# Kernel tuning notes

Measured on AMD Instinct MI355X. Metric: run time of the kernel, lower is better.

The kernel has to match this reference:

```python
import jax, jax.numpy as jnp
import numpy as np

EPS = 1e-07


def _pairwise_iou_xyxy(pred, tgt):
    # pred: [P,4], tgt: [T,4] in (x1,y1,x2,y2) form -> [P,T] IoU
    lt = jnp.maximum(pred[:, None, :2], tgt[None, :, :2])   # [P,T,2]
    rb = jnp.minimum(pred[:, None, 2:], tgt[None, :, 2:])   # [P,T,2]
    wh = jnp.clip(rb - lt, 0.0)                             # [P,T,2]
    inter = wh[..., 0] * wh[..., 1]                         # [P,T]
    pa = (pred[:, 2] - pred[:, 0]) * (pred[:, 3] - pred[:, 1])  # [P]
    ta = (tgt[:, 2] - tgt[:, 0]) * (tgt[:, 3] - tgt[:, 1])      # [T]
    union = pa[:, None] + ta[None, :] - inter
    return inter / (union + EPS)


def setup_inputs() -> dict:
    key = jax.random.key(0)
    k1, k2 = jax.random.split(key)
    pred_boxes = jax.random.uniform(k1, (8192, 4), dtype=jnp.float32)
    target_boxes = jax.random.uniform(k2, (4096, 4), dtype=jnp.float32)
    return {"pred_boxes": pred_boxes, "target_boxes": target_boxes}


def reference(pred_boxes, target_boxes):
    num_preds = pred_boxes.shape[0]
    num_targets = target_boxes.shape[0]
    if num_preds != num_targets:
        pairwise_ious = _pairwise_iou_xyxy(pred_boxes, target_boxes)  # [P,T]
        indices = jnp.argmax(pairwise_ious, axis=1)                    # [P]
        target_boxes = target_boxes[indices]                           # [P,4]

    # DIoU part interprets boxes as (cx, cy, w, h) -- faithful to the original
    pred_centers, pred_sizes = pred_boxes[:, :2], pred_boxes[:, 2:]
    tgt_centers, tgt_sizes = target_boxes[:, :2], target_boxes[:, 2:]

    pred_lt = pred_centers - pred_sizes / 2
    pred_rb = pred_centers + pred_sizes / 2
    tgt_lt = tgt_centers - tgt_sizes / 2
    tgt_rb = tgt_centers + tgt_sizes / 2

    inter_wh = jnp.clip(jnp.minimum(pred_rb, tgt_rb) - jnp.maximum(pred_lt, tgt_lt), 0.0)
    inter_area = inter_wh[:, 0] * inter_wh[:, 1]
    pred_area = pred_sizes[:, 0] * pred_sizes[:, 1]
    tgt_area = tgt_sizes[:, 0] * tgt_sizes[:, 1]
    iou = inter_area / (pred_area + tgt_area - inter_area + EPS)

    center_distance = jnp.sum((pred_centers - tgt_centers) ** 2, axis=1)
    enc_wh = jnp.maximum(pred_rb, tgt_rb) - jnp.minimum(pred_lt, tgt_lt)
    enc_diag = jnp.sum(enc_wh ** 2, axis=1)

    diou = iou - center_distance / (enc_diag + EPS)
    return 1.0 - jnp.mean(diou)
```

## Files before the change

kernel.cpp:

```cpp
#include <hip/hip_runtime.h>

#define EPS 1e-7f

constexpr int NPRED  = 8192;
constexpr int NTGT   = 4096;
constexpr int BLOCK  = 256;
constexpr int PW     = 4;
constexpr int PPB    = 16;
constexpr int TSPLIT = 8;
constexpr int TCHUNK = NTGT / TSPLIT;
constexpr int GRID_P = NPRED / PPB;
constexpr int GRID   = GRID_P * TSPLIT;

__device__ __forceinline__ unsigned sortable_key(float f) {
  unsigned b = __float_as_uint(f);
  return (b & 0x80000000u) ? ~b : (b | 0x80000000u);
}

__global__ __launch_bounds__(BLOCK, 8)
void diou_argmax(const float4* __restrict__ pred,
                 const float4* __restrict__ tgt,
                 unsigned long long* __restrict__ pk) {
  __shared__ float4 sT[TCHUNK];
  const int lane  = threadIdx.x & 63;
  const int wave  = threadIdx.x >> 6;
  const int pblk  = blockIdx.x % GRID_P;
  const int tq    = blockIdx.x / GRID_P;
  const int tbase = tq * TCHUNK;
  const int pbase = pblk * PPB + wave * PW;

  for (int t = threadIdx.x; t < TCHUNK; t += BLOCK) sT[t] = tgt[tbase + t];

  float4 p[PW];
  float  paeps[PW];
  float  bestV[PW];
  int    bestI[PW];
#pragma unroll
  for (int i = 0; i < PW; ++i) {
    p[i]     = pred[pbase + i];
    paeps[i] = (p[i].z - p[i].x) * (p[i].w - p[i].y) + EPS;
    bestV[i] = -INFINITY;
    bestI[i] = 0;
  }
  __syncthreads();

#pragma unroll 4
  for (int t0 = 0; t0 < TCHUNK; t0 += 64) {
    const int t = t0 + lane;
    float4 tb = sT[t];
    float  ta = (tb.z - tb.x) * (tb.w - tb.y);
#pragma unroll
    for (int i = 0; i < PW; ++i) {
      float w = fminf(p[i].z, tb.z) - fmaxf(p[i].x, tb.x);
      float h = fminf(p[i].w, tb.w) - fmaxf(p[i].y, tb.y);
      w = fmaxf(w, 0.f);
      h = fmaxf(h, 0.f);
      float inter = w * h;
      float denom = (paeps[i] + ta) - inter;
      float iou   = inter * __builtin_amdgcn_rcpf(denom);
      iou += 0.0f;
      if (iou > bestV[i]) { bestV[i] = iou; bestI[i] = t; }
    }
  }

#pragma unroll
  for (int i = 0; i < PW; ++i) {
    float v  = bestV[i];
    int   ix = bestI[i];
    for (int off = 32; off > 0; off >>= 1) {
      float ov = __shfl_down(v, off, 64);
      int   oi = __shfl_down(ix, off, 64);
      if (ov > v || (ov == v && oi < ix)) { v = ov; ix = oi; }
    }
    if (lane == 0) {
      unsigned long long packed =
          ((unsigned long long)sortable_key(v) << 32) |
          (unsigned)(NTGT - 1 - (tbase + ix));
      atomicMax(&pk[pbase + i], packed);
    }
  }
}

__global__ __launch_bounds__(1024)
void diou_gather_finalize(const float4* __restrict__ pred,
                          const float4* __restrict__ tgt,
                          const unsigned long long* __restrict__ pk,
                          float* __restrict__ out) {
  __shared__ float sP[16];
  const int tid  = threadIdx.x;
  const int lane = tid & 63;

  float v = 0.f;
  for (int j = tid; j < NPRED; j += 1024) {
    float4 p  = pred[j];
    int    ix = NTGT - 1 - (int)(unsigned)(pk[j] & 0xFFFFFFFFu);
    float4 t  = tgt[ix];

    float phw = 0.5f * p.z, phh = 0.5f * p.w;
    float thw = 0.5f * t.z, thh = 0.5f * t.w;
    float pltx = p.x - phw, plty = p.y - phh;
    float prbx = p.x + phw, prby = p.y + phh;
    float tltx = t.x - thw, tlty = t.y - thh;
    float trbx = t.x + thw, trby = t.y + thh;

    float iw = fmaxf(fminf(prbx, trbx) - fmaxf(pltx, tltx), 0.f);
    float ih = fmaxf(fminf(prby, trby) - fmaxf(plty, tlty), 0.f);
    float inter = iw * ih;
    float parea = p.z * p.w;
    float tarea = t.z * t.w;
    float iou   = inter / (parea + tarea - inter + EPS);

    float dx = p.x - t.x, dy = p.y - t.y;
    float cd = dx * dx + dy * dy;

    float ew = fmaxf(prbx, trbx) - fminf(pltx, tltx);
    float eh = fmaxf(prby, trby) - fminf(plty, tlty);
    float diag = ew * ew + eh * eh;

    v += iou - cd / (diag + EPS);
  }

  for (int off = 32; off > 0; off >>= 1) v += __shfl_down(v, off, 64);
  if (lane == 0) sP[tid >> 6] = v;
  __syncthreads();
  if (tid == 0) {
    float s = 0.f;
#pragma unroll
    for (int i = 0; i < 16; ++i) s += sP[i];
    out[0] = 1.f - s * (1.f / (float)NPRED);
  }
}

extern "C" void kernel_launch(void* const* d_in, const int* in_sizes, int n_in,
                              void* d_out, int out_size, void* d_ws, size_t ws_size,
                              hipStream_t stream) {
  const float4* pred = (const float4*)d_in[0];
  const float4* tgt  = (const float4*)d_in[1];
  unsigned long long* pk = (unsigned long long*)d_ws;

  hipMemsetAsync(pk, 0, NPRED * sizeof(unsigned long long), stream);
  diou_argmax<<<GRID, BLOCK, 0, stream>>>(pred, tgt, pk);
  diou_gather_finalize<<<1, 1024, 0, stream>>>(pred, tgt, pk, (float*)d_out);
}
```

Measured before the change: 83.57 us.

## Fuse argmax with DIoU gather, drop target split and atomics

```diff
diff --git a/kernel.cpp b/kernel.cpp
--- a/kernel.cpp
+++ b/kernel.cpp
@@ -2,100 +2,65 @@
 
 #define EPS 1e-7f
 
-constexpr int NPRED  = 8192;
-constexpr int NTGT   = 4096;
-constexpr int BLOCK  = 256;
-constexpr int PW     = 4;
-constexpr int PPB    = 16;
-constexpr int TSPLIT = 8;
-constexpr int TCHUNK = NTGT / TSPLIT;
-constexpr int GRID_P = NPRED / PPB;
-constexpr int GRID   = GRID_P * TSPLIT;
-
-__device__ __forceinline__ unsigned sortable_key(float f) {
-  unsigned b = __float_as_uint(f);
-  return (b & 0x80000000u) ? ~b : (b | 0x80000000u);
-}
+constexpr int NPRED = 8192;
+constexpr int NTGT  = 4096;
+constexpr int BLOCK = 512;
+constexpr int PPB   = 8;
+constexpr int GRID  = NPRED / PPB;
+constexpr int CH    = 1024;
+constexpr int NCH   = NTGT / CH;
 
 __global__ __launch_bounds__(BLOCK, 8)
-void diou_argmax(const float4* __restrict__ pred,
-                 const float4* __restrict__ tgt,
-                 unsigned long long* __restrict__ pk) {
-  __shared__ float4 sT[TCHUNK];
-  const int lane  = threadIdx.x & 63;
-  const int wave  = threadIdx.x >> 6;
-  const int pblk  = blockIdx.x % GRID_P;
-  const int tq    = blockIdx.x / GRID_P;
-  const int tbase = tq * TCHUNK;
-  const int pbase = pblk * PPB + wave * PW;
+void diou_main(const float4* __restrict__ pred,
+               const float4* __restrict__ tgt,
+               float* __restrict__ partial) {
+  __shared__ float4 sT[CH];
+  __shared__ float  sA[CH];
+  __shared__ float  sP[PPB];
+  const int lane = threadIdx.x & 63;
+  const int wave = threadIdx.x >> 6;
+  const int pidx = blockIdx.x * PPB + wave;
 
-  for (int t = threadIdx.x; t < TCHUNK; t += BLOCK) sT[t] = tgt[tbase + t];
+  const float4 p = pred[pidx];
+  const float paeps = (p.z - p.x) * (p.w - p.y) + EPS;
 
-  float4 p[PW];
-  float  paeps[PW];
-  float  bestV[PW];
-  int    bestI[PW];
-#pragma unroll
-  for (int i = 0; i < PW; ++i) {
-    p[i]     = pred[pbase + i];
-    paeps[i] = (p[i].z - p[i].x) * (p[i].w - p[i].y) + EPS;
-    bestV[i] = -INFINITY;
-    bestI[i] = 0;
-  }
-  __syncthreads();
+  float bestV = -INFINITY;
+  int   bestB = 0;
 
+  for (int c = 0; c < NCH; ++c) {
+    __syncthreads();
+    for (int t = threadIdx.x; t < CH; t += BLOCK) {
+      float4 tb = tgt[c * CH + t];
+      sT[t] = tb;
+      sA[t] = (tb.z - tb.x) * (tb.w - tb.y);
+    }
+    __syncthreads();
+    const int cb = c * CH;
 #pragma unroll 4
-  for (int t0 = 0; t0 < TCHUNK; t0 += 64) {
-    const int t = t0 + lane;
-    float4 tb = sT[t];
-    float  ta = (tb.z - tb.x) * (tb.w - tb.y);
-#pragma unroll
-    for (int i = 0; i < PW; ++i) {
-      float w = fminf(p[i].z, tb.z) - fmaxf(p[i].x, tb.x);
-      float h = fminf(p[i].w, tb.w) - fmaxf(p[i].y, tb.y);
+    for (int t0 = 0; t0 < CH; t0 += 64) {
+      float4 tb = sT[t0 + lane];
+      float  ta = sA[t0 + lane];
+      float w = fminf(p.z, tb.z) - fmaxf(p.x, tb.x);
+      float h = fminf(p.w, tb.w) - fmaxf(p.y, tb.y);
       w = fmaxf(w, 0.f);
       h = fmaxf(h, 0.f);
       float inter = w * h;
-      float denom = (paeps[i] + ta) - inter;
-      float iou   = inter * __builtin_amdgcn_rcpf(denom);
-      iou += 0.0f;
-      if (iou > bestV[i]) { bestV[i] = iou; bestI[i] = t; }
+      float den   = (paeps + ta) - inter;
+      float iou   = inter * __builtin_amdgcn_rcpf(den);
+      if (iou > bestV) { bestV = iou; bestB = cb + t0; }
     }
   }
 
-#pragma unroll
-  for (int i = 0; i < PW; ++i) {
-    float v  = bestV[i];
-    int   ix = bestI[i];
-    for (int off = 32; off > 0; off >>= 1) {
-      float ov = __shfl_down(v, off, 64);
-      int   oi = __shfl_down(ix, off, 64);
-      if (ov > v || (ov == v && oi < ix)) { v = ov; ix = oi; }
-    }
-    if (lane == 0) {
-      unsigned long long packed =
-          ((unsigned long long)sortable_key(v) << 32) |
-          (unsigned)(NTGT - 1 - (tbase + ix));
-      atomicMax(&pk[pbase + i], packed);
-    }
+  int   ix = bestB + lane;
+  float v  = bestV;
+  for (int off = 32; off > 0; off >>= 1) {
+    float ov = __shfl_down(v, off, 64);
+    int   oi = __shfl_down(ix, off, 64);
+    if (ov > v || (ov == v && oi < ix)) { v = ov; ix = oi; }
   }
-}
 
-__global__ __launch_bounds__(1024)
-void diou_gather_finalize(const float4* __restrict__ pred,
-                          const float4* __restrict__ tgt,
-                          const unsigned long long* __restrict__ pk,
-                          float* __restrict__ out) {
-  __shared__ float sP[16];
-  const int tid  = threadIdx.x;
-  const int lane = tid & 63;
-
-  float v = 0.f;
-  for (int j = tid; j < NPRED; j += 1024) {
-    float4 p  = pred[j];
-    int    ix = NTGT - 1 - (int)(unsigned)(pk[j] & 0xFFFFFFFFu);
-    float4 t  = tgt[ix];
-
+  if (lane == 0) {
+    float4 t = tgt[ix];
     float phw = 0.5f * p.z, phh = 0.5f * p.w;
     float thw = 0.5f * t.z, thh = 0.5f * t.w;
     float pltx = p.x - phw, plty = p.y - phh;
@@ -117,16 +82,31 @@
     float eh = fmaxf(prby, trby) - fminf(plty, tlty);
     float diag = ew * ew + eh * eh;
 
-    v += iou - cd / (diag + EPS);
+    sP[wave] = iou - cd / (diag + EPS);
   }
+  __syncthreads();
+  if (threadIdx.x == 0) {
+    float s = 0.f;
+#pragma unroll
+    for (int i = 0; i < PPB; ++i) s += sP[i];
+    partial[blockIdx.x] = s;
+  }
+}
 
+__global__ __launch_bounds__(1024)
+void diou_finalize(const float* __restrict__ partial,
+                   float* __restrict__ out) {
+  __shared__ float sW[16];
+  const int tid  = threadIdx.x;
+  const int lane = tid & 63;
+  float v = partial[tid];
   for (int off = 32; off > 0; off >>= 1) v += __shfl_down(v, off, 64);
-  if (lane == 0) sP[tid >> 6] = v;
+  if (lane == 0) sW[tid >> 6] = v;
   __syncthreads();
   if (tid == 0) {
     float s = 0.f;
 #pragma unroll
-    for (int i = 0; i < 16; ++i) s += sP[i];
+    for (int i = 0; i < 16; ++i) s += sW[i];
     out[0] = 1.f - s * (1.f / (float)NPRED);
   }
 }
@@ -136,9 +116,8 @@
                               hipStream_t stream) {
   const float4* pred = (const float4*)d_in[0];
   const float4* tgt  = (const float4*)d_in[1];
-  unsigned long long* pk = (unsigned long long*)d_ws;
+  float* partial = (float*)d_ws;
 
-  hipMemsetAsync(pk, 0, NPRED * sizeof(unsigned long long), stream);
-  diou_argmax<<<GRID, BLOCK, 0, stream>>>(pred, tgt, pk);
-  diou_gather_finalize<<<1, 1024, 0, stream>>>(pred, tgt, pk, (float*)d_out);
+  diou_main<<<GRID, BLOCK, 0, stream>>>(pred, tgt, partial);
+  diou_finalize<<<1, 1024, 0, stream>>>(partial, (float*)d_out);
 }
```

Result: faster. 77.18 us (-7.6%).
